# Kernel tuning notes

Measured on AMD Instinct MI355X. Metric: run time of the kernel, lower is better.

The kernel has to match this reference:

```python
import jax, jax.numpy as jnp
import numpy as np

R = 80   # volume_reso
B, NV, C, H, W = 1, 4, 32, 64, 64


def _voxel_grid():
    line = np.linspace(-1.0, 1.0, R)
    x, y, z = np.meshgrid(line, line, line, indexing='ij')
    return jnp.asarray(np.stack([x, y, z]).reshape(3, -1), dtype=jnp.float32)  # (3, R^3)


def grid_sample_pix(img, coords):
    """Bilinear sample at pixel coords (align_corners=True convention, zero padding).
    img: (BN, C, H, W); coords: (BN, N, 2) as (x, y) in pixel units.
    Returns vals (BN, C, N) and in-bounds mask (BN, N)."""
    BN, Cc, Hh, Ww = img.shape
    x, y = coords[..., 0], coords[..., 1]
    mask = ((x >= 0) & (x <= Ww - 1) & (y >= 0) & (y <= Hh - 1)).astype(img.dtype)
    x0 = jnp.floor(x); y0 = jnp.floor(y)
    x1 = x0 + 1.0;     y1 = y0 + 1.0
    wx1 = x - x0; wx0 = 1.0 - wx1
    wy1 = y - y0; wy0 = 1.0 - wy1
    imgf = img.reshape(BN, Cc, Hh * Ww)

    def corner(xi, yi, w):
        valid = ((xi >= 0) & (xi <= Ww - 1) & (yi >= 0) & (yi <= Hh - 1)).astype(img.dtype)
        xc = jnp.clip(xi, 0, Ww - 1).astype(jnp.int32)
        yc = jnp.clip(yi, 0, Hh - 1).astype(jnp.int32)
        flat = yc * Ww + xc                                   # (BN, N)
        vals = jnp.take_along_axis(imgf, flat[:, None, :], axis=2)  # (BN, C, N)
        return vals * (valid * w)[:, None, :]

    out = (corner(x0, y0, wx0 * wy0) + corner(x1, y0, wx1 * wy0)
           + corner(x0, y1, wx0 * wy1) + corner(x1, y1, wx1 * wy1))
    return out, mask


def setup_inputs() -> dict:
    key = jax.random.key(0)
    ks = jax.random.split(key, 7)
    feats = jax.random.normal(ks[0], (B, NV, C, H, W), dtype=jnp.float32)
    # structured pinhole projection matrices (K @ w2c embedded in 4x4)
    f = 55.0; cx = (W - 1) / 2.0; cy = (H - 1) / 2.0
    poses = np.zeros((B, NV, 4, 4), np.float32)
    for v in range(NV):
        poses[0, v] = np.array([[f, 0, cx, 0.0],
                                [0, f, cy, 0.1 * v],
                                [0, 0, 1.0, 3.0 + 0.2 * v],
                                [0, 0, 0, 1.0]], np.float32)
    return {
        'feats': feats,
        'source_poses': jnp.asarray(poses),
        'W1': jax.random.normal(ks[1], (32, 32), jnp.float32) / np.sqrt(32.0),
        'b1': jax.random.normal(ks[2], (32,), jnp.float32) * 0.01,
        'W2': jax.random.normal(ks[3], (32, 16), jnp.float32) / np.sqrt(32.0),
        'b2': jax.random.normal(ks[4], (16,), jnp.float32) * 0.01,
        'W3': jax.random.normal(ks[5], (16, 8), jnp.float32) / np.sqrt(16.0),
        'b3': jax.random.normal(ks[6], (8,), jnp.float32) * 0.01,
    }


def reference(feats, source_poses, W1, b1, W2, b2, W3, b3):
    N = R ** 3
    xyz = _voxel_grid()                                             # (3, N)
    homo = jnp.concatenate([xyz, jnp.ones((1, N), xyz.dtype)], 0)   # (4, N)
    proj = jnp.einsum('bvij,jn->bvin', source_poses, homo)[:, :, :3]  # (B,NV,3,N)
    z = proj[:, :, 2]                                               # (B,NV,N)
    mask_valid_depth = (z > 0).astype(feats.dtype)
    uv = proj[:, :, :2] / proj[:, :, 2:3]                           # (B,NV,2,N)
    coords = jnp.transpose(uv, (0, 1, 3, 2)).reshape(B * NV, N, 2)
    vals, mask = grid_sample_pix(feats.reshape(B * NV, C, H, W), coords)
    vf = jnp.transpose(vals.reshape(B, NV, C, N), (0, 1, 3, 2))     # (B,NV,N,C)
    mask = mask.reshape(B, NV, N) * mask_valid_depth                # (B,NV,N)
    weight = mask / (jnp.sum(mask, axis=1, keepdims=True) + 1e-8)
    # small MLP 32 -> 32 -> 16 -> 8
    h = jax.nn.relu(vf @ W1 + b1)
    h = jax.nn.relu(h @ W2 + b2)
    h = h @ W3 + b3                                                 # (B,NV,N,8)
    w = weight[..., None]
    mean = jnp.sum(h * w, axis=1, keepdims=True)                    # (B,1,N,8)
    var = jnp.sum(w * (h - mean) ** 2, axis=1)                      # (B,N,8)
    mv = jnp.concatenate([mean[:, 0], var], axis=-1)                # (B,N,16)
    vol = mv.reshape(B, R, R, R, 16)                                # (B,X,Y,Z,16)
    return jnp.transpose(vol, (0, 4, 3, 2, 1))                      # (B,16,Z,Y,X)
```

## Files before the change

kernel.cpp:

```cpp
#include <hip/hip_runtime.h>
#include <cstddef>

#define RR 80
#define NVIEW 4
#define CH 32
#define IH 64
#define IW 64
#define NPIX (IH*IW)
#define NVOX (RR*RR*RR)

#define PLANE_H (NPIX*8)
#define VIEW_H  (4*PLANE_H)

typedef _Float16 half4_t  __attribute__((ext_vector_type(4)));
typedef _Float16 half8_t  __attribute__((ext_vector_type(8)));
typedef float    float4_t __attribute__((ext_vector_type(4)));

__global__ __launch_bounds__(256) void g_precompute(
    const float* __restrict__ feats, const float* __restrict__ W1,
    _Float16* __restrict__ G)
{
    int g = blockIdx.x >> 6;
    int p = (blockIdx.x & 63)*256 + threadIdx.x;
    __shared__ float sW1[CH*8];
    if (threadIdx.x < CH*8) {
        int ic = threadIdx.x >> 3, e = threadIdx.x & 7;
        sW1[threadIdx.x] = W1[ic*CH + 8*g + e];
    }
    __syncthreads();
    int v  = p >> 12;
    int yx = p & 4095;
    const float* fb = feats + ((size_t)v*CH)*NPIX + yx;
    float acc[8];
    #pragma unroll
    for (int e=0;e<8;++e) acc[e] = 0.f;
    #pragma unroll
    for (int ic=0; ic<CH; ++ic) {
        float fv = fb[(size_t)ic*NPIX];
        #pragma unroll
        for (int e=0;e<8;++e) acc[e] = fmaf(fv, sW1[ic*8+e], acc[e]);
    }
    half8_t h;
    #pragma unroll
    for (int e=0;e<8;++e) h[e] = (_Float16)acc[e];
    *(half8_t*)(G + (size_t)v*VIEW_H + (size_t)g*PLANE_H + (size_t)yx*8) = h;
}

__global__ __launch_bounds__(256) void dgfv_main(
    const _Float16* __restrict__ G,
    const float* __restrict__ poses,
    const float* __restrict__ b1,
    const float* __restrict__ W2, const float* __restrict__ b2,
    const float* __restrict__ W3, const float* __restrict__ b3,
    float* __restrict__ out)
{
    const int wid  = threadIdx.x >> 6;
    const int lane = threadIdx.x & 63;
    const int lq   = lane >> 4;
    const int lc   = lane & 15;
    const int vbase = blockIdx.x*256 + wid*64 + lc;

    half8_t w2a;
    #pragma unroll
    for (int j=0;j<8;++j) w2a[j] = (_Float16)W2[(lq*8+j)*16 + lc];
    half4_t w3a;
    #pragma unroll
    for (int j=0;j<4;++j) w3a[j] = (_Float16)W3[(lq*4+j)*8 + (lc&7)];
    float4_t c1init, c2init;
    #pragma unroll
    for (int r=0;r<4;++r) {
        c1init[r] = b2[lq*4+r];
        c2init[r] = b3[(lq*4+r)&7];
    }
    half8_t b1h;
    #pragma unroll
    for (int j=0;j<8;++j) b1h[j] = (_Float16)b1[8*lq+j];

    const float step = 2.0f/(float)(RR-1);

    #pragma unroll
    for (int p=0;p<4;++p) {
        int vx = vbase + 16*p;
        int i  = vx % RR;
        int t  = vx / RR;
        int j_ = t % RR;
        int k_ = t / RR;
        float x = fmaf((float)i,  step, -1.0f);
        float y = fmaf((float)j_, step, -1.0f);
        float z = fmaf((float)k_, step, -1.0f);

        float accA[4], accB[4], accM = 0.f;
        #pragma unroll
        for (int r=0;r<4;++r) { accA[r]=0.f; accB[r]=0.f; }

        #pragma unroll
        for (int v = 0; v < NVIEW; ++v) {
            const float* P = poses + v*16;
            float px = fmaf(P[0],x, fmaf(P[1],y, fmaf(P[2], z, P[3])));
            float py = fmaf(P[4],x, fmaf(P[5],y, fmaf(P[6], z, P[7])));
            float pz = fmaf(P[8],x, fmaf(P[9],y, fmaf(P[10],z, P[11])));
            float r0 = __builtin_amdgcn_rcpf(pz);
            r0 = r0*(2.0f - pz*r0);
            float u  = px*r0;
            float w  = py*r0;

            float mk = (pz > 0.f && u >= 0.f && u <= (float)(IW-1)
                                  && w >= 0.f && w <= (float)(IH-1)) ? 1.f : 0.f;

            float uc = fminf(fmaxf(u, 0.f), (float)(IW-1));
            float wc = fminf(fmaxf(w, 0.f), (float)(IH-1));
            float fx0 = floorf(uc), fy0 = floorf(wc);
            float tx = uc - fx0, ty = wc - fy0;
            int x0 = (int)fx0, y0 = (int)fy0;
            float wx0 = 1.f - tx, wy0 = 1.f - ty;

            _Float16 w00h = (_Float16)(wx0*wy0), w10h = (_Float16)(tx*wy0);
            _Float16 w01h = (_Float16)(wx0*ty),  w11h = (_Float16)(tx*ty);

            const _Float16* base = G + (size_t)v*VIEW_H + (size_t)lq*PLANE_H
                                     + (size_t)(y0*IW + x0)*8;
            half8_t a = *(const half8_t*)(base);
            half8_t b = *(const half8_t*)(base + 8);
            half8_t c = *(const half8_t*)(base + IW*8);
            half8_t d = *(const half8_t*)(base + IW*8 + 8);
            half8_t h1 = a*w00h + b*w10h + c*w01h + d*w11h + b1h;
            h1 = __builtin_elementwise_max(h1, (half8_t)(_Float16)0.f);

            float4_t d1 = __builtin_amdgcn_mfma_f32_16x16x32_f16(w2a, h1, c1init, 0,0,0);
            half4_t h2;
            #pragma unroll
            for (int r=0;r<4;++r) h2[r] = (_Float16)fmaxf(d1[r], 0.f);

            float4_t d2 = __builtin_amdgcn_mfma_f32_16x16x16f16(w3a, h2, c2init, 0,0,0);

            #pragma unroll
            for (int r=0;r<4;++r) {
                float h3 = d2[r];
                float tt = mk*h3;
                accA[r] += tt;
                accB[r]  = fmaf(tt, h3, accB[r]);
            }
            accM += mk;
        }

        float S   = accM + 1e-8f;
        float inv = 1.f/S;
        float sw  = accM*inv;
        #pragma unroll
        for (int r=0;r<4;++r) {
            float mean = accA[r]*inv;
            float var  = fmaf(-mean*mean, (2.f - sw), accB[r]*inv);
            float val  = (lq < 2) ? mean : var;
            int   cch  = 4*lq + r;
            out[(size_t)cch*NVOX + vx] = val;
        }
    }
}

extern "C" void kernel_launch(void* const* d_in, const int* in_sizes, int n_in,
                              void* d_out, int out_size, void* d_ws, size_t ws_size,
                              hipStream_t stream)
{
    const float* feats = (const float*)d_in[0];
    const float* poses = (const float*)d_in[1];
    const float* W1    = (const float*)d_in[2];
    const float* b1    = (const float*)d_in[3];
    const float* W2    = (const float*)d_in[4];
    const float* b2    = (const float*)d_in[5];
    const float* W3    = (const float*)d_in[6];
    const float* b3    = (const float*)d_in[7];
    float* out = (float*)d_out;

    _Float16* G = (_Float16*)d_ws;
    g_precompute<<<256, 256, 0, stream>>>(feats, W1, G);
    dgfv_main<<<NVOX/256, 256, 0, stream>>>(G, poses, b1, W2, b2, W3, b3, out);
}
```

Baseline: 103.4 us.

## Compute per-voxel projection once per lane and share via ds_bpermute

Previously each lane recomputed the projection, bilinear weights and mask for voxels that four lane groups (lq) shared, so the same work ran four times. Now each of the 64 lanes projects its own voxel once per view. Packed weights, offset and mask bits are then sent to the lanes that consume them with ds_bpermute, and the view loop becomes the outer loop. This trades redundant VALU work for cross-lane permute traffic and 32 accumulators per lane, which raises register pressure. The offset is packed into 16 bits with the mask in the sign bit.

```diff
diff --git a/kernel.cpp b/kernel.cpp
--- a/kernel.cpp
+++ b/kernel.cpp
@@ -12,6 +12,7 @@
 #define PLANE_H (NPIX*8)
 #define VIEW_H  (4*PLANE_H)
 
+typedef _Float16 half2_t  __attribute__((ext_vector_type(2)));
 typedef _Float16 half4_t  __attribute__((ext_vector_type(4)));
 typedef _Float16 half8_t  __attribute__((ext_vector_type(8)));
 typedef float    float4_t __attribute__((ext_vector_type(4)));
@@ -58,7 +59,8 @@
     const int lane = threadIdx.x & 63;
     const int lq   = lane >> 4;
     const int lc   = lane & 15;
-    const int vbase = blockIdx.x*256 + wid*64 + lc;
+    const int vbase0 = blockIdx.x*256 + wid*64;
+    const int vown   = vbase0 + lane;
 
     half8_t w2a;
     #pragma unroll
@@ -76,54 +78,67 @@
     #pragma unroll
     for (int j=0;j<8;++j) b1h[j] = (_Float16)b1[8*lq+j];
 
+    {
+    }
+    int io  = vown % RR;
+    int to  = vown / RR;
+    int jo  = to % RR;
+    int ko  = to / RR;
     const float step = 2.0f/(float)(RR-1);
+    const float xo = fmaf((float)io, step, -1.0f);
+    const float yo = fmaf((float)jo, step, -1.0f);
+    const float zo = fmaf((float)ko, step, -1.0f);
 
+    float accA[16], accB[16];
     #pragma unroll
-    for (int p=0;p<4;++p) {
-        int vx = vbase + 16*p;
-        int i  = vx % RR;
-        int t  = vx / RR;
-        int j_ = t % RR;
-        int k_ = t / RR;
-        float x = fmaf((float)i,  step, -1.0f);
-        float y = fmaf((float)j_, step, -1.0f);
-        float z = fmaf((float)k_, step, -1.0f);
+    for (int q=0;q<16;++q) { accA[q]=0.f; accB[q]=0.f; }
+    float accMown = 0.f;
 
-        float accA[4], accB[4], accM = 0.f;
-        #pragma unroll
-        for (int r=0;r<4;++r) { accA[r]=0.f; accB[r]=0.f; }
+    for (int v = 0; v < NVIEW; ++v) {
+        const float* P = poses + v*16;
+        float px = fmaf(P[0],xo, fmaf(P[1],yo, fmaf(P[2], zo, P[3])));
+        float py = fmaf(P[4],xo, fmaf(P[5],yo, fmaf(P[6], zo, P[7])));
+        float pz = fmaf(P[8],xo, fmaf(P[9],yo, fmaf(P[10],zo, P[11])));
+        float r0 = __builtin_amdgcn_rcpf(pz);
+        r0 = r0*(2.0f - pz*r0);
+        float u  = px*r0;
+        float w  = py*r0;
+        bool mko = (pz > 0.f && u >= 0.f && u <= (float)(IW-1)
+                              && w >= 0.f && w <= (float)(IH-1));
+        accMown += mko ? 1.f : 0.f;
+
+        float uc = fminf(fmaxf(u, 0.f), (float)(IW-1));
+        float wc = fminf(fmaxf(w, 0.f), (float)(IH-1));
+        float fx0 = floorf(uc), fy0 = floorf(wc);
+        float tx = uc - fx0, ty = wc - fy0;
+        int x0 = (int)fx0, y0 = (int)fy0;
+        float wx0 = 1.f - tx, wy0 = 1.f - ty;
+
+        half2_t wpA = { (_Float16)(wx0*wy0), (_Float16)(tx*wy0) };
+        half2_t wpB = { (_Float16)(wx0*ty),  (_Float16)(tx*ty)  };
+        int pk0 = __builtin_bit_cast(int, wpA);
+        int pk1 = __builtin_bit_cast(int, wpB);
+        int pk2 = ((y0*IW + x0)*8) | (mko ? (int)0x80000000 : 0);
+
+        const _Float16* gp = G + (size_t)v*VIEW_H + (size_t)lq*PLANE_H;
 
         #pragma unroll
-        for (int v = 0; v < NVIEW; ++v) {
-            const float* P = poses + v*16;
-            float px = fmaf(P[0],x, fmaf(P[1],y, fmaf(P[2], z, P[3])));
-            float py = fmaf(P[4],x, fmaf(P[5],y, fmaf(P[6], z, P[7])));
-            float pz = fmaf(P[8],x, fmaf(P[9],y, fmaf(P[10],z, P[11])));
-            float r0 = __builtin_amdgcn_rcpf(pz);
-            r0 = r0*(2.0f - pz*r0);
-            float u  = px*r0;
-            float w  = py*r0;
+        for (int p=0;p<4;++p) {
+            int addr = (16*p + lc) << 2;
+            int s0 = __builtin_amdgcn_ds_bpermute(addr, pk0);
+            int s1 = __builtin_amdgcn_ds_bpermute(addr, pk1);
+            int s2 = __builtin_amdgcn_ds_bpermute(addr, pk2);
+            half2_t wA = __builtin_bit_cast(half2_t, s0);
+            half2_t wB = __builtin_bit_cast(half2_t, s1);
+            int offp   = s2 & 0xFFFF;
+            float mkf  = (float)((unsigned)s2 >> 31);
 
-            float mk = (pz > 0.f && u >= 0.f && u <= (float)(IW-1)
-                                  && w >= 0.f && w <= (float)(IH-1)) ? 1.f : 0.f;
-
-            float uc = fminf(fmaxf(u, 0.f), (float)(IW-1));
-            float wc = fminf(fmaxf(w, 0.f), (float)(IH-1));
-            float fx0 = floorf(uc), fy0 = floorf(wc);
-            float tx = uc - fx0, ty = wc - fy0;
-            int x0 = (int)fx0, y0 = (int)fy0;
-            float wx0 = 1.f - tx, wy0 = 1.f - ty;
-
-            _Float16 w00h = (_Float16)(wx0*wy0), w10h = (_Float16)(tx*wy0);
-            _Float16 w01h = (_Float16)(wx0*ty),  w11h = (_Float16)(tx*ty);
-
-            const _Float16* base = G + (size_t)v*VIEW_H + (size_t)lq*PLANE_H
-                                     + (size_t)(y0*IW + x0)*8;
+            const _Float16* base = gp + offp;
             half8_t a = *(const half8_t*)(base);
             half8_t b = *(const half8_t*)(base + 8);
             half8_t c = *(const half8_t*)(base + IW*8);
             half8_t d = *(const half8_t*)(base + IW*8 + 8);
-            half8_t h1 = a*w00h + b*w10h + c*w01h + d*w11h + b1h;
+            half8_t h1 = a*wA[0] + b*wA[1] + c*wB[0] + d*wB[1] + b1h;
             h1 = __builtin_elementwise_max(h1, (half8_t)(_Float16)0.f);
 
             float4_t d1 = __builtin_amdgcn_mfma_f32_16x16x32_f16(w2a, h1, c1init, 0,0,0);
@@ -136,23 +151,29 @@
             #pragma unroll
             for (int r=0;r<4;++r) {
                 float h3 = d2[r];
-                float tt = mk*h3;
-                accA[r] += tt;
-                accB[r]  = fmaf(tt, h3, accB[r]);
+                float tt = mkf*h3;
+                accA[4*p+r] += tt;
+                accB[4*p+r]  = fmaf(tt, h3, accB[4*p+r]);
             }
-            accM += mk;
         }
+    }
 
+    int accMi = __builtin_bit_cast(int, accMown);
+    #pragma unroll
+    for (int p=0;p<4;++p) {
+        int addr = (16*p + lc) << 2;
+        float accM = __builtin_bit_cast(float,
+                        __builtin_amdgcn_ds_bpermute(addr, accMi));
         float S   = accM + 1e-8f;
         float inv = 1.f/S;
         float sw  = accM*inv;
         #pragma unroll
         for (int r=0;r<4;++r) {
-            float mean = accA[r]*inv;
-            float var  = fmaf(-mean*mean, (2.f - sw), accB[r]*inv);
+            float mean = accA[4*p+r]*inv;
+            float var  = fmaf(-mean*mean, (2.f - sw), accB[4*p+r]*inv);
             float val  = (lq < 2) ? mean : var;
             int   cch  = 4*lq + r;
-            out[(size_t)cch*NVOX + vx] = val;
+            out[(size_t)cch*NVOX + vbase0 + 16*p + lc] = val;
         }
     }
 }
```

After: 106.3 us. 1.03x slower.
